# Performance work log

Hardware: AMD Instinct MI355X
Metric: run time of the kernel (lower is better)

The kernel has to match this reference:

```python
import jax, jax.numpy as jnp
import numpy as np

WEIGHT_BIT = 8
BIAS_BIT = 32
STRIDE = (1, 1)
PAD = ((1, 1), (1, 1))


def setup_inputs() -> dict:
    key = jax.random.key(0)
    k1, k2, k3, k4 = jax.random.split(key, 4)
    N, Cin, Cout, K, H, W = 64, 256, 256, 3, 28, 28
    x_q = jax.random.randint(k1, (N, Cin, H, W), 0, 255, dtype=jnp.int32)
    scale_x = jax.random.uniform(k2, (1,), dtype=jnp.float32) * 0.1 + 0.01
    weight = jax.random.normal(k3, (Cout, Cin, K, K), dtype=jnp.float32) * 0.05
    bias = jax.random.normal(k4, (Cout,), dtype=jnp.float32) * 0.1
    return {"x_q": x_q, "scale_x": scale_x, "weight": weight, "bias": bias}


def _quant_weight_per_channel(w, bit):
    # symmetric per-output-channel quantization from min/max (ZeroQ SymmetricQuantFunction)
    n = 2 ** (bit - 1) - 1  # 127 for 8-bit
    wf = w.reshape(w.shape[0], -1)
    sat = jnp.maximum(jnp.abs(wf.min(axis=1)), jnp.abs(wf.max(axis=1)))
    scale = jnp.clip(sat, 1e-8, None) / n  # [Cout]
    w_q = jnp.clip(jnp.round(w / scale[:, None, None, None]), -n - 1, n).astype(jnp.int32)
    return w_q, scale


def reference(x_q, scale_x, weight, bias):
    # fake-quantize weight per output channel
    w_q, scale_w = _quant_weight_per_channel(weight, WEIGHT_BIT)  # int32 [Cout,Cin,K,K], f32 [Cout]
    scale_out = scale_w * scale_x[0]  # [Cout]
    # quantize bias with the combined scale (bias_bit=32)
    nb = float(2 ** (BIAS_BIT - 1) - 1)
    b_q = jnp.clip(jnp.round(bias / scale_out), -nb - 1.0, nb).astype(jnp.int32)  # [Cout]
    out_q = jax.lax.conv_general_dilated(
        x_q, w_q, window_strides=STRIDE, padding=PAD,
        dimension_numbers=("NCHW", "OIHW", "NCHW"),
    ) + b_q[None, :, None, None]
    return out_q, scale_out.reshape(1, -1, 1, 1)
```

## Files before the change

kernel.cpp:

```cpp
#include <hip/hip_runtime.h>
#include <hip/hip_bf16.h>

typedef int   i32x4 __attribute__((ext_vector_type(4)));

#define N_IMG 64
#define CIN   256
#define COUT  256
#define HH    28
#define WW    28
#define PH    30
#define PW    30
#define M_TOT (N_IMG*HH*WW)
#define OUT_ELEMS (N_IMG*COUT*HH*WW)

#define XT_BYTES   ((size_t)N_IMG*PH*PW*CIN)
#define WT_OFF     (XT_BYTES)
#define WT_BYTES   ((size_t)9*COUT*CIN)
#define BQ_OFF     (WT_OFF + WT_BYTES)

#define GLD16(g, l) __builtin_amdgcn_global_load_lds( \
    (const __attribute__((address_space(1))) void*)(g), \
    (__attribute__((address_space(3))) void*)(l), 16, 0, 0)

__global__ __launch_bounds__(256) void transform_x(const int* __restrict__ xq,
                                                   signed char* __restrict__ xt) {
    __shared__ int xs[CIN*29];
    const int b = blockIdx.x;
    const int n = b / PH, py = b % PH;
    const int t = threadIdx.x;
    signed char* dst = xt + ((size_t)(n*PH + py))*PW*CIN;
    if (py == 0 || py == PH-1) {
        for (int i = t; i < PW*CIN; i += 256) dst[i] = -127;
        return;
    }
    const int h = py - 1;
    const int* src = xq + (size_t)n*CIN*HH*WW + h*WW;
    for (int i = t; i < CIN*WW; i += 256) {
        const int ci = i / WW, w = i % WW;
        xs[ci*29 + w] = src[ci*HH*WW + w];
    }
    __syncthreads();
    for (int i = t; i < PW*CIN; i += 256) {
        const int px = i / CIN, ci = i % CIN;
        const int v = (px == 0 || px == PW-1) ? 0 : xs[ci*29 + (px-1)];
        dst[px*CIN + ci] = (signed char)(v - 127);
    }
}

__global__ __launch_bounds__(256) void quant_w(const float* __restrict__ weight,
                                               const float* __restrict__ scale_x,
                                               const float* __restrict__ bias,
                                               signed char* __restrict__ wt,
                                               int* __restrict__ bq,
                                               float* __restrict__ out_tail) {
    __shared__ float red[256];
    __shared__ int  sred[256];
    const int co = blockIdx.x, t = threadIdx.x;
    const float* wrow = weight + (size_t)co*CIN*9;
    float wv[9];
    float mx = 0.f;
    for (int it = 0; it < 9; ++it) {
        float v = wrow[it*256 + t];
        wv[it] = v;
        mx = fmaxf(mx, fabsf(v));
    }
    red[t] = mx;
    __syncthreads();
    for (int s = 128; s > 0; s >>= 1) {
        if (t < s) red[t] = fmaxf(red[t], red[t+s]);
        __syncthreads();
    }
    const float scale = fmaxf(red[0], 1e-8f) / 127.f;
    int isum = 0;
    for (int it = 0; it < 9; ++it) {
        const int i = it*256 + t;
        const int ci = i / 9, rs = i % 9;
        float q = rintf(wv[it] / scale);
        q = fminf(fmaxf(q, -128.f), 127.f);
        const int qi = (int)q;
        isum += qi;
        wt[(size_t)rs*COUT*CIN + co*CIN + ci] = (signed char)qi;
    }
    sred[t] = isum;
    __syncthreads();
    for (int s = 128; s > 0; s >>= 1) {
        if (t < s) sred[t] += sred[t+s];
        __syncthreads();
    }
    if (t == 0) {
        const float so = scale * scale_x[0];
        out_tail[co] = so;
        bq[co] = (int)rintf(bias[co] / so) + 127 * sred[0];
    }
}

__global__ __launch_bounds__(512, 1) void conv_mfma(const signed char* __restrict__ xt,
                                                    const signed char* __restrict__ wt,
                                                    const int* __restrict__ bq,
                                                    float* __restrict__ out) {
    __shared__ signed char Ash[2*32768];
    __shared__ signed char Bsh[2*16384];
    const int d = threadIdx.x;
    const int w8 = d >> 6;
    const int lane = d & 63, lr = lane & 15, kg = lane >> 4;
    const int wm = w8 >> 1, wn = w8 & 1;
    const int bx = blockIdx.x;
    const int mb = (bx & 7)*49 + (bx >> 3);
    const int m0 = mb << 7;

    const int srow = d >> 3;
    const int skc  = (d & 7) ^ (srow & 7);
    const signed char* aS = wt + srow*CIN + (skc << 4);
    const signed char* bS0;
    const signed char* bS1;
    {
        int m = m0 + srow;
        int n = m / 784, hw = m % 784, h = hw / 28, wq = hw % 28;
        bS0 = xt + ((size_t)((n*PH + h)*PW + wq))*CIN + (skc << 4);
        m += 64;
        n = m / 784; hw = m % 784; h = hw / 28; wq = hw % 28;
        bS1 = xt + ((size_t)((n*PH + h)*PW + wq))*CIN + (skc << 4);
    }
    const int w8off = w8 << 10;

    i32x4 acc[4][4] = {};

    const int a0 = (wm*64 + lr)*128 + ((kg ^ (lr & 7)) << 4);
    const int b0 = (wn*64 + lr)*128 + ((kg ^ (lr & 7)) << 4);

#define STAGE(T_, P_) do { \
    const int tap_ = (T_) >> 1, c_ = (T_) & 1; \
    const int r3_ = (tap_*171) >> 9; \
    const int ao_ = tap_*(COUT*CIN) + (c_ << 7); \
    const int bo_ = ((r3_*PW + (tap_ - r3_*3)) << 8) + (c_ << 7); \
    GLD16(aS + ao_,         Ash + (P_)*32768 +         w8off); \
    GLD16(aS + ao_ + 16384, Ash + (P_)*32768 +  8192 + w8off); \
    GLD16(aS + ao_ + 32768, Ash + (P_)*32768 + 16384 + w8off); \
    GLD16(aS + ao_ + 49152, Ash + (P_)*32768 + 24576 + w8off); \
    GLD16(bS0 + bo_,        Bsh + (P_)*16384 +         w8off); \
    GLD16(bS1 + bo_,        Bsh + (P_)*16384 +  8192 + w8off); \
} while (0)

#define COMPUTE(P_) do { \
    const signed char* A_ = Ash + (P_)*32768; \
    const signed char* B_ = Bsh + (P_)*16384; \
    _Pragma("unroll") \
    for (int ks = 0; ks < 2; ++ks) { \
        const int ar = a0 ^ (ks << 6); \
        const int br = b0 ^ (ks << 6); \
        i32x4 af[4], bf[4]; \
        _Pragma("unroll") \
        for (int mr = 0; mr < 4; ++mr) \
            af[mr] = *(const i32x4*)&A_[ar + mr*2048]; \
        _Pragma("unroll") \
        for (int nr = 0; nr < 4; ++nr) \
            bf[nr] = *(const i32x4*)&B_[br + nr*2048]; \
        _Pragma("unroll") \
        for (int mr = 0; mr < 4; ++mr) \
            _Pragma("unroll") \
            for (int nr = 0; nr < 4; ++nr) \
                acc[mr][nr] = __builtin_amdgcn_mfma_i32_16x16x64_i8( \
                    af[mr], bf[nr], acc[mr][nr], 0, 0, 0); \
    } \
} while (0)

#define SYNCPT() do { \
    asm volatile("s_waitcnt vmcnt(0) lgkmcnt(0)" ::: "memory"); \
    __builtin_amdgcn_s_barrier(); \
    __builtin_amdgcn_sched_barrier(0); \
} while (0)

    STAGE(0, 0);
#pragma unroll 1
    for (int tt = 0; tt < 18; tt += 2) {
        SYNCPT();
        STAGE(tt + 1, 1);
        COMPUTE(0);
        SYNCPT();
        if (tt < 16) STAGE(tt + 2, 0);
        COMPUTE(1);
    }

#pragma unroll
    for (int nr = 0; nr < 4; ++nr) {
        const int mm = m0 + wn*64 + nr*16 + lr;
        const int nn = mm / 784, hw2 = mm % 784;
        float* orow = out + (size_t)nn*COUT*784 + hw2;
#pragma unroll
        for (int mr = 0; mr < 4; ++mr) {
            const int co = wm*64 + mr*16 + kg*4;
#pragma unroll
            for (int rg = 0; rg < 4; ++rg)
                orow[(size_t)(co + rg)*784] = (float)(acc[mr][nr][rg] + bq[co + rg]);
        }
    }
#undef STAGE
#undef COMPUTE
#undef SYNCPT
}

extern "C" void kernel_launch(void* const* d_in, const int* in_sizes, int n_in,
                              void* d_out, int out_size, void* d_ws, size_t ws_size,
                              hipStream_t stream) {
    const int*   xq      = (const int*)d_in[0];
    const float* scale_x = (const float*)d_in[1];
    const float* weight  = (const float*)d_in[2];
    const float* bias    = (const float*)d_in[3];
    float* out = (float*)d_out;

    signed char* xt = (signed char*)d_ws;
    signed char* wt = (signed char*)((char*)d_ws + WT_OFF);
    int*         bq = (int*)((char*)d_ws + BQ_OFF);

    hipLaunchKernelGGL(transform_x, dim3(N_IMG*PH), dim3(256), 0, stream, xq, xt);
    hipLaunchKernelGGL(quant_w, dim3(COUT), dim3(256), 0, stream,
                       weight, scale_x, bias, wt, bq, out + OUT_ELEMS);
    hipLaunchKernelGGL(conv_mfma, dim3(M_TOT/128), dim3(512), 0, stream,
                       xt, wt, bq, out);
}
```

Measured before the change: 76.17 us.

## Split conv output channels across grid y with 256-thread blocks, two per CU

The conv kernel's block tile shrinks from 256x128 to 128x128: Cout is split over a second grid dimension and each block runs 4 waves instead of 8. Shared memory per block halves, so launch bounds now allow two blocks per CU, and the grid doubles to improve occupancy and wave balance across CUs. In exchange, each activation tile is loaded twice (once per Cout half), which raises global and L2 traffic for the im2col-style B loads.

```diff
diff --git a/kernel.cpp b/kernel.cpp
--- a/kernel.cpp
+++ b/kernel.cpp
@@ -94,34 +94,32 @@
     }
 }
 
-__global__ __launch_bounds__(512, 1) void conv_mfma(const signed char* __restrict__ xt,
+__global__ __launch_bounds__(256, 2) void conv_mfma(const signed char* __restrict__ xt,
                                                     const signed char* __restrict__ wt,
                                                     const int* __restrict__ bq,
                                                     float* __restrict__ out) {
-    __shared__ signed char Ash[2*32768];
+    __shared__ signed char Ash[2*16384];
     __shared__ signed char Bsh[2*16384];
     const int d = threadIdx.x;
-    const int w8 = d >> 6;
+    const int w4 = d >> 6;
     const int lane = d & 63, lr = lane & 15, kg = lane >> 4;
-    const int wm = w8 >> 1, wn = w8 & 1;
+    const int wm = w4 >> 1, wn = w4 & 1;
     const int bx = blockIdx.x;
     const int mb = (bx & 7)*49 + (bx >> 3);
     const int m0 = mb << 7;
+    const int co0 = blockIdx.y << 7;
 
     const int srow = d >> 3;
     const int skc  = (d & 7) ^ (srow & 7);
-    const signed char* aS = wt + srow*CIN + (skc << 4);
-    const signed char* bS0;
-    const signed char* bS1;
-    {
-        int m = m0 + srow;
-        int n = m / 784, hw = m % 784, h = hw / 28, wq = hw % 28;
-        bS0 = xt + ((size_t)((n*PH + h)*PW + wq))*CIN + (skc << 4);
-        m += 64;
-        n = m / 784; hw = m % 784; h = hw / 28; wq = hw % 28;
-        bS1 = xt + ((size_t)((n*PH + h)*PW + wq))*CIN + (skc << 4);
-    }
-    const int w8off = w8 << 10;
+    const signed char* aS = wt + (size_t)(co0 + srow)*CIN + (skc << 4);
+    const signed char* bS[4];
+#pragma unroll
+    for (int j = 0; j < 4; ++j) {
+        const int m = m0 + srow + j*32;
+        const int n = m / 784, hw = m % 784, h = hw / 28, wq = hw % 28;
+        bS[j] = xt + ((size_t)((n*PH + h)*PW + wq))*CIN + (skc << 4);
+    }
+    const int w4off = w4 << 10;
 
     i32x4 acc[4][4] = {};
 
@@ -133,16 +131,18 @@
     const int r3_ = (tap_*171) >> 9; \
     const int ao_ = tap_*(COUT*CIN) + (c_ << 7); \
     const int bo_ = ((r3_*PW + (tap_ - r3_*3)) << 8) + (c_ << 7); \
-    GLD16(aS + ao_,         Ash + (P_)*32768 +         w8off); \
-    GLD16(aS + ao_ + 16384, Ash + (P_)*32768 +  8192 + w8off); \
-    GLD16(aS + ao_ + 32768, Ash + (P_)*32768 + 16384 + w8off); \
-    GLD16(aS + ao_ + 49152, Ash + (P_)*32768 + 24576 + w8off); \
-    GLD16(bS0 + bo_,        Bsh + (P_)*16384 +         w8off); \
-    GLD16(bS1 + bo_,        Bsh + (P_)*16384 +  8192 + w8off); \
+    GLD16(aS + ao_,         Ash + (P_)*16384 +         w4off); \
+    GLD16(aS + ao_ +  8192, Ash + (P_)*16384 +  4096 + w4off); \
+    GLD16(aS + ao_ + 16384, Ash + (P_)*16384 +  8192 + w4off); \
+    GLD16(aS + ao_ + 24576, Ash + (P_)*16384 + 12288 + w4off); \
+    GLD16(bS[0] + bo_,      Bsh + (P_)*16384 +         w4off); \
+    GLD16(bS[1] + bo_,      Bsh + (P_)*16384 +  4096 + w4off); \
+    GLD16(bS[2] + bo_,      Bsh + (P_)*16384 +  8192 + w4off); \
+    GLD16(bS[3] + bo_,      Bsh + (P_)*16384 + 12288 + w4off); \
 } while (0)
 
 #define COMPUTE(P_) do { \
-    const signed char* A_ = Ash + (P_)*32768; \
+    const signed char* A_ = Ash + (P_)*16384; \
     const signed char* B_ = Bsh + (P_)*16384; \
     _Pragma("unroll") \
     for (int ks = 0; ks < 2; ++ks) { \
@@ -188,7 +188,7 @@
         float* orow = out + (size_t)nn*COUT*784 + hw2;
 #pragma unroll
         for (int mr = 0; mr < 4; ++mr) {
-            const int co = wm*64 + mr*16 + kg*4;
+            const int co = co0 + wm*64 + mr*16 + kg*4;
 #pragma unroll
             for (int rg = 0; rg < 4; ++rg)
                 orow[(size_t)(co + rg)*784] = (float)(acc[mr][nr][rg] + bq[co + rg]);
@@ -215,6 +215,6 @@
     hipLaunchKernelGGL(transform_x, dim3(N_IMG*PH), dim3(256), 0, stream, xq, xt);
     hipLaunchKernelGGL(quant_w, dim3(COUT), dim3(256), 0, stream,
                        weight, scale_x, bias, wt, bq, out + OUT_ELEMS);
-    hipLaunchKernelGGL(conv_mfma, dim3(M_TOT/128), dim3(512), 0, stream,
+    hipLaunchKernelGGL(conv_mfma, dim3(M_TOT/128, COUT/128), dim3(256), 0, stream,
                        xt, wt, bq, out);
 }
```

After: 73.13 us. 4.0% less time.
